# Optimization experiments

Hardware: AMD Instinct MI355X
Metric: run time of the kernel (lower is better)

The kernel has to match this reference:

```python
import jax, jax.numpy as jnp
import numpy as np

N_USERS = 50000
N_ITEMS = 50000
E = 400000
S = 128   # in_feats_s (memory / GRU hidden)
T = 64    # in_feats_t (time encoding dim)
ED = 64   # edge feature dim
M = 2 * S + T + ED  # in_feats_m = 384

_BASIS_FREQ = jnp.asarray(1.0 / 10 ** np.linspace(0, 9, T), dtype=jnp.float32)


def time_encode(ts):
    # cos(ts * freq + phase), phase == 0
    return jnp.cos(ts[:, None] * _BASIS_FREQ[None, :])


def mean_message(src_mem, dst_mem, ts, e, src, dst, n_dst):
    # mail per edge: [E, 2S + T + ED]
    mail = jnp.concatenate(
        [src_mem[src], dst_mem[dst], time_encode(ts), e], axis=1)
    s = jax.ops.segment_sum(mail, dst, num_segments=n_dst)
    cnt = jax.ops.segment_sum(jnp.ones_like(ts), dst, num_segments=n_dst)
    return s / jnp.maximum(cnt, 1.0)[:, None]


def gru_step(x, h, w_ih, w_hh, b_ih, b_hh):
    # single-step PyTorch GRU; gate order r, z, n
    gi = x @ w_ih.T + b_ih
    gh = h @ w_hh.T + b_hh
    ir, iz, i_n = jnp.split(gi, 3, axis=1)
    hr, hz, h_n = jnp.split(gh, 3, axis=1)
    r = jax.nn.sigmoid(ir + hr)
    z = jax.nn.sigmoid(iz + hz)
    n = jnp.tanh(i_n + r * h_n)
    return (1.0 - z) * n + z * h


def setup_inputs() -> dict:
    key = jax.random.key(0)
    ks = jax.random.split(key, 16)
    sc = 1.0 / np.sqrt(S)
    return {
        "si":   jax.random.normal(ks[0], (N_USERS, S), jnp.float32),
        "sj":   jax.random.normal(ks[1], (N_ITEMS, S), jnp.float32),
        "si_r": jax.random.normal(ks[2], (N_ITEMS, S), jnp.float32),
        "sj_r": jax.random.normal(ks[3], (N_USERS, S), jnp.float32),
        "t":    jax.random.uniform(ks[4], (E,), jnp.float32),
        "t_r":  jax.random.uniform(ks[5], (E,), jnp.float32),
        "e":    jax.random.normal(ks[6], (E, ED), jnp.float32),
        "e_r":  jax.random.normal(ks[7], (E, ED), jnp.float32),
        "w_ih": jax.random.normal(ks[8], (3 * S, M), jnp.float32) * sc,
        "w_hh": jax.random.normal(ks[9], (3 * S, S), jnp.float32) * sc,
        "b_ih": jax.random.normal(ks[10], (3 * S,), jnp.float32) * sc,
        "b_hh": jax.random.normal(ks[11], (3 * S,), jnp.float32) * sc,
        "src_g":  jax.random.randint(ks[12], (E,), 0, N_USERS, jnp.int32),
        "dst_g":  jax.random.randint(ks[13], (E,), 0, N_ITEMS, jnp.int32),
        "src_gr": jax.random.randint(ks[14], (E,), 0, N_ITEMS, jnp.int32),
        "dst_gr": jax.random.randint(ks[15], (E,), 0, N_USERS, jnp.int32),
    }


def reference(si, sj, si_r, sj_r, t, t_r, e, e_r,
              w_ih, w_hh, b_ih, b_hh,
              src_g, dst_g, src_gr, dst_gr):
    # g: user -> item; g_r: item -> user
    mj = mean_message(si, sj, t, e, src_g, dst_g, N_ITEMS)       # messages to items
    mi = mean_message(si_r, sj_r, t_r, e_r, src_gr, dst_gr, N_USERS)  # messages to users
    si_out = gru_step(mi, sj_r, w_ih, w_hh, b_ih, b_hh)  # user memory update
    sj_out = gru_step(mj, sj, w_ih, w_hh, b_ih, b_hh)    # item memory update
    return (si_out, sj_out)
```

## Files before the change

### kernel.cpp

```cpp
#include <hip/hip_runtime.h>
#include <math.h>

#define NUSERS 50000
#define NITEMS 50000
#define NTOT   100000
#define NNODE  50000
#define NCHUNK 196
#define MTILES 6250
#define KDIM   512

typedef __attribute__((ext_vector_type(4))) float f32x4;
typedef __attribute__((ext_vector_type(8))) short short8;
typedef unsigned int u32;

#define AS1 __attribute__((address_space(1)))
#define AS3 __attribute__((address_space(3)))

static __device__ __forceinline__ unsigned short f2bf(float f) {
  unsigned int u = __float_as_uint(f);
  u += 0x7fffu + ((u >> 16) & 1u);
  return (unsigned short)(u >> 16);
}

static __device__ __forceinline__ u32 pack2(float x, float y) {
  return (u32)f2bf(x) | ((u32)f2bf(y) << 16);
}

static __device__ __forceinline__ void gload_lds16(const void* g, void* l) {
  __builtin_amdgcn_global_load_lds((const AS1 u32*)g, (AS3 u32*)l, 16, 0, 0);
}

__global__ void pack_w_kernel(const float* __restrict__ w_ih,
                              const float* __restrict__ w_hh,
                              const float* __restrict__ b_ih,
                              const float* __restrict__ b_hh,
                              unsigned short* __restrict__ Wb,
                              float* __restrict__ bb) {
  int idx = blockIdx.x * 256 + threadIdx.x;
  int j = idx & 7, l = (idx >> 3) & 63, ktt = idx >> 9;
  int kt = ktt & 15, tt = ktt >> 4;
  int g = tt * 16 + (l & 15);
  int k = kt * 32 + (l >> 4) * 8 + j;
  float v;
  if (g < 256)      v = (k < 384) ? w_ih[g * 384 + k] : w_hh[g * 128 + (k - 384)];
  else if (g < 384) v = (k < 384) ? w_ih[g * 384 + k] : 0.0f;
  else              v = (k < 384) ? 0.0f : w_hh[(g - 128) * 128 + (k - 384)];
  Wb[idx] = f2bf(v);
  if (idx < 512) {
    float b = (idx < 256) ? (b_ih[idx] + b_hh[idx])
            : (idx < 384) ? b_ih[idx]
                          : b_hh[idx - 128];
    bb[idx] = b;
  }
}

__global__ void cast_mem_kernel(const float* __restrict__ si,
                                const float* __restrict__ si_r,
                                unsigned short* __restrict__ si_b,
                                unsigned short* __restrict__ sir_b) {
  int i = blockIdx.x * 256 + threadIdx.x;
  const float* src; unsigned short* dst; int off;
  if (i < 800000) { src = si;   dst = si_b;  off = i; }
  else            { src = si_r; dst = sir_b; off = i - 800000; }
  const f32x4* p = (const f32x4*)(src + (size_t)off * 8);
  f32x4 a = p[0], b = p[1];
  short8 o;
  o[0] = f2bf(a[0]); o[1] = f2bf(a[1]); o[2] = f2bf(a[2]); o[3] = f2bf(a[3]);
  o[4] = f2bf(b[0]); o[5] = f2bf(b[1]); o[6] = f2bf(b[2]); o[7] = f2bf(b[3]);
  *(short8*)(dst + (size_t)off * 8) = o;
}

__global__ void hist_kernel(const int* __restrict__ dst_g,
                            const int* __restrict__ dst_gr,
                            int* __restrict__ deg_j, int* __restrict__ deg_i, int E) {
  int i = blockIdx.x * 256 + threadIdx.x;
  if (i < E) atomicAdd(&deg_j[dst_g[i]], 1);
  else if (i < 2 * E) atomicAdd(&deg_i[dst_gr[i - E]], 1);
}

__global__ void chunksum_kernel(const int* __restrict__ deg_j,
                                const int* __restrict__ deg_i,
                                int* __restrict__ csum) {
  int c = blockIdx.x;
  const int* deg = (c < NCHUNK) ? deg_j : deg_i;
  int cc = (c < NCHUNK) ? c : c - NCHUNK;
  int t = threadIdx.x;
  int idx = cc * 256 + t;
  int v = (idx < NNODE) ? deg[idx] : 0;
  for (int off = 32; off; off >>= 1) v += __shfl_down(v, off, 64);
  __shared__ int wsum[4];
  if ((t & 63) == 0) wsum[t >> 6] = v;
  __syncthreads();
  if (t == 0) csum[c] = wsum[0] + wsum[1] + wsum[2] + wsum[3];
}

__global__ void chunkscan_kernel(const int* __restrict__ csum, int* __restrict__ coff) {
  int d = blockIdx.x;
  const int* cs = csum + d * NCHUNK;
  int* co = coff + d * NCHUNK;
  int t = threadIdx.x, lane = t & 63, w = t >> 6;
  int v = (t < NCHUNK) ? cs[t] : 0;
  int x = v;
  for (int off = 1; off < 64; off <<= 1) {
    int y = __shfl_up(x, off, 64);
    if (lane >= off) x += y;
  }
  __shared__ int wt[4];
  if (lane == 63) wt[w] = x;
  __syncthreads();
  int add = 0;
  for (int k = 0; k < 4; ++k) if (k < w) add += wt[k];
  if (t < NCHUNK) co[t] = add + x - v;
}

__global__ void localscan_kernel(const int* __restrict__ deg_j,
                                 const int* __restrict__ deg_i,
                                 const int* __restrict__ coff,
                                 int* __restrict__ rs_j, int* __restrict__ cur_j,
                                 int* __restrict__ rs_i, int* __restrict__ cur_i) {
  int c = blockIdx.x;
  bool dj = c < NCHUNK;
  const int* deg = dj ? deg_j : deg_i;
  int cc = dj ? c : c - NCHUNK;
  int* rs = dj ? rs_j : rs_i;
  int* cur = dj ? cur_j : cur_i;
  int base = coff[c];
  int t = threadIdx.x, lane = t & 63, w = t >> 6;
  int idx = cc * 256 + t;
  int v = (idx < NNODE) ? deg[idx] : 0;
  int x = v;
  for (int off = 1; off < 64; off <<= 1) {
    int y = __shfl_up(x, off, 64);
    if (lane >= off) x += y;
  }
  __shared__ int wt[4];
  if (lane == 63) wt[w] = x;
  __syncthreads();
  int add = 0;
  for (int k = 0; k < 4; ++k) if (k < w) add += wt[k];
  int ex = base + add + x - v;
  if (idx < NNODE) { rs[idx] = ex; cur[idx] = ex; }
}

__global__ void fill_kernel(const int* __restrict__ src_g, const int* __restrict__ dst_g,
                            const float* __restrict__ t,
                            const int* __restrict__ src_gr, const int* __restrict__ dst_gr,
                            const float* __restrict__ t_r,
                            int* __restrict__ cur_j, int* __restrict__ cur_i,
                            int4* __restrict__ recP_j, int4* __restrict__ recP_i,
                            int E) {
  int i = blockIdx.x * 256 + threadIdx.x;
  if (i < E) {
    int pos = atomicAdd(&cur_j[dst_g[i]], 1);
    recP_j[pos] = make_int4(src_g[i], i, __float_as_int(t[i]), 0);
  } else if (i < 2 * E) {
    int k = i - E;
    int pos = atomicAdd(&cur_i[dst_gr[k]], 1);
    recP_i[pos] = make_int4(src_gr[k], k, __float_as_int(t_r[k]), 0);
  }
}

__global__ __launch_bounds__(256) void gather_kernel(
    const unsigned short* __restrict__ si_b, const unsigned short* __restrict__ sir_b,
    const float* __restrict__ sj, const float* __restrict__ sj_r,
    const float* __restrict__ e, const float* __restrict__ e_r,
    const int* __restrict__ rs_j, const int* __restrict__ rs_i,
    const int* __restrict__ deg_j, const int* __restrict__ deg_i,
    const int4* __restrict__ recP_j, const int4* __restrict__ recP_i,
    unsigned short* __restrict__ Xb) {
  __shared__ __align__(16) unsigned short rowbuf[4][512];
  int wid = threadIdx.x >> 6, lane = threadIdx.x & 63;
  int node = blockIdx.x * 4 + wid;
  bool user = node < NUSERS;
  int idx = user ? node : node - NUSERS;
  const unsigned short* smem = user ? sir_b : si_b;
  const float* h    = user ? sj_r : sj;
  const float* ef   = user ? e_r : e;
  int start = __builtin_amdgcn_readfirstlane((user ? rs_i : rs_j)[idx]);
  int deg   = __builtin_amdgcn_readfirstlane((user ? deg_i : deg_j)[idx]);
  const int4* rec = user ? recP_i : recP_j;

  float freq = __expf((float)lane * -0.3289407276f);
  float2 hvf = *(const float2*)(h + (size_t)idx * 128 + 2 * lane);

  float asx = 0.f, asy = 0.f;
  float at  = 0.f;
  float ae  = 0.f;

  for (int base = 0; base < deg; base += 64) {
    int nn = deg - base; if (nn > 64) nn = 64;
    int cl = (lane < nn) ? base + lane : base + nn - 1;
    int4 r = rec[start + cl];
    for (int j0 = 0; j0 < nn; j0 += 8) {
      int j1 = (j0 + 1 < nn) ? j0 + 1 : nn - 1;
      int j2 = (j0 + 2 < nn) ? j0 + 2 : nn - 1;
      int j3 = (j0 + 3 < nn) ? j0 + 3 : nn - 1;
      int j4 = (j0 + 4 < nn) ? j0 + 4 : nn - 1;
      int j5 = (j0 + 5 < nn) ? j0 + 5 : nn - 1;
      int j6 = (j0 + 6 < nn) ? j0 + 6 : nn - 1;
      int j7 = (j0 + 7 < nn) ? j0 + 7 : nn - 1;
      float w1 = (j0 + 1 < nn) ? 1.0f : 0.0f;
      float w2 = (j0 + 2 < nn) ? 1.0f : 0.0f;
      float w3 = (j0 + 3 < nn) ? 1.0f : 0.0f;
      float w4 = (j0 + 4 < nn) ? 1.0f : 0.0f;
      float w5 = (j0 + 5 < nn) ? 1.0f : 0.0f;
      float w6 = (j0 + 6 < nn) ? 1.0f : 0.0f;
      float w7 = (j0 + 7 < nn) ? 1.0f : 0.0f;

      int s0 = __builtin_amdgcn_readlane(r.x, j0), e0 = __builtin_amdgcn_readlane(r.y, j0);
      int s1 = __builtin_amdgcn_readlane(r.x, j1), e1 = __builtin_amdgcn_readlane(r.y, j1);
      int s2 = __builtin_amdgcn_readlane(r.x, j2), e2 = __builtin_amdgcn_readlane(r.y, j2);
      int s3 = __builtin_amdgcn_readlane(r.x, j3), e3 = __builtin_amdgcn_readlane(r.y, j3);
      int s4 = __builtin_amdgcn_readlane(r.x, j4), e4 = __builtin_amdgcn_readlane(r.y, j4);
      int s5 = __builtin_amdgcn_readlane(r.x, j5), e5 = __builtin_amdgcn_readlane(r.y, j5);
      int s6 = __builtin_amdgcn_readlane(r.x, j6), e6 = __builtin_amdgcn_readlane(r.y, j6);
      int s7 = __builtin_amdgcn_readlane(r.x, j7), e7 = __builtin_amdgcn_readlane(r.y, j7);

      u32 v0 = *(const u32*)(smem + ((size_t)s0 << 7) + 2 * lane);
      u32 v1 = *(const u32*)(smem + ((size_t)s1 << 7) + 2 * lane);
      u32 v2 = *(const u32*)(smem + ((size_t)s2 << 7) + 2 * lane);
      u32 v3 = *(const u32*)(smem + ((size_t)s3 << 7) + 2 * lane);
      u32 v4 = *(const u32*)(smem + ((size_t)s4 << 7) + 2 * lane);
      u32 v5 = *(const u32*)(smem + ((size_t)s5 << 7) + 2 * lane);
      u32 v6 = *(const u32*)(smem + ((size_t)s6 << 7) + 2 * lane);
      u32 v7 = *(const u32*)(smem + ((size_t)s7 << 7) + 2 * lane);
      float f0 = ef[((size_t)e0 << 6) + lane];
      float f1 = ef[((size_t)e1 << 6) + lane];
      float f2 = ef[((size_t)e2 << 6) + lane];
      float f3 = ef[((size_t)e3 << 6) + lane];
      float f4 = ef[((size_t)e4 << 6) + lane];
      float f5 = ef[((size_t)e5 << 6) + lane];
      float f6 = ef[((size_t)e6 << 6) + lane];
      float f7 = ef[((size_t)e7 << 6) + lane];

      float c0 = __cosf(__int_as_float(__builtin_amdgcn_readlane(r.z, j0)) * freq);
      float c1 = __cosf(__int_as_float(__builtin_amdgcn_readlane(r.z, j1)) * freq);
      float c2 = __cosf(__int_as_float(__builtin_amdgcn_readlane(r.z, j2)) * freq);
      float c3 = __cosf(__int_as_float(__builtin_amdgcn_readlane(r.z, j3)) * freq);
      float c4 = __cosf(__int_as_float(__builtin_amdgcn_readlane(r.z, j4)) * freq);
      float c5 = __cosf(__int_as_float(__builtin_amdgcn_readlane(r.z, j5)) * freq);
      float c6 = __cosf(__int_as_float(__builtin_amdgcn_readlane(r.z, j6)) * freq);
      float c7 = __cosf(__int_as_float(__builtin_amdgcn_readlane(r.z, j7)) * freq);

      float l0 = __uint_as_float(v0 << 16), g0 = __uint_as_float(v0 & 0xffff0000u);
      float l1 = __uint_as_float(v1 << 16), g1 = __uint_as_float(v1 & 0xffff0000u);
      float l2 = __uint_as_float(v2 << 16), g2 = __uint_as_float(v2 & 0xffff0000u);
      float l3 = __uint_as_float(v3 << 16), g3 = __uint_as_float(v3 & 0xffff0000u);
      float l4 = __uint_as_float(v4 << 16), g4 = __uint_as_float(v4 & 0xffff0000u);
      float l5 = __uint_as_float(v5 << 16), g5 = __uint_as_float(v5 & 0xffff0000u);
      float l6 = __uint_as_float(v6 << 16), g6 = __uint_as_float(v6 & 0xffff0000u);
      float l7 = __uint_as_float(v7 << 16), g7 = __uint_as_float(v7 & 0xffff0000u);

      asx += l0 + w1 * l1 + w2 * l2 + w3 * l3 + w4 * l4 + w5 * l5 + w6 * l6 + w7 * l7;
      asy += g0 + w1 * g1 + w2 * g2 + w3 * g3 + w4 * g4 + w5 * g5 + w6 * g6 + w7 * g7;
      at  += c0 + w1 * c1 + w2 * c2 + w3 * c3 + w4 * c4 + w5 * c5 + w6 * c6 + w7 * c7;
      ae  += f0 + w1 * f1 + w2 * f2 + w3 * f3 + w4 * f4 + w5 * f5 + w6 * f6 + w7 * f7;
    }
  }

  float invc = (deg > 0) ? 1.0f / (float)deg : 0.0f;
  float hz   = (deg > 0) ? 1.0f : 0.0f;

  unsigned short* rb = rowbuf[wid];
  u32* rb32 = (u32*)rb;
  rb32[lane]       = pack2(asx * invc, asy * invc);
  rb32[64 + lane]  = pack2(hvf.x * hz, hvf.y * hz);
  rb[256 + lane]   = f2bf(at * invc);
  rb[320 + lane]   = f2bf(ae * invc);
  rb32[192 + lane] = pack2(hvf.x, hvf.y);

  int rt = node >> 4, m = node & 15;
  int kt2 = lane >> 2, q2 = lane & 3;
  short8 vv = *(const short8*)(rb + lane * 8);
  *(short8*)(Xb + (((size_t)rt * 16 + kt2) * 64 + q2 * 16 + m) * 8) = vv;
}

__global__ __launch_bounds__(1024, 4) void gemm_gru_kernel(
    const unsigned short* __restrict__ Xb,
    const unsigned short* __restrict__ Wb,
    const float* __restrict__ bb,
    const float* __restrict__ sj_r,
    const float* __restrict__ sj,
    float* __restrict__ out) {
  __shared__ __align__(16) unsigned short sA[32768];
  __shared__ __align__(16) unsigned short sW[2][16384];
  int wid = threadIdx.x >> 6, lane = threadIdx.x & 63;
  int mg = wid >> 3, cg = wid & 7;
  int mbase = blockIdx.x * 4;
  int col16 = lane & 15, quad = lane >> 4;

  f32x4 acc[2][4];
#pragma unroll
  for (int mi = 0; mi < 2; ++mi)
#pragma unroll
    for (int g = 0; g < 4; ++g) acc[mi][g] = (f32x4)0.0f;

#pragma unroll
  for (int i = 0; i < 4; ++i) {
    int u = wid * 4 + i;
    int mt = mbase + (u >> 4);
    if (mt >= MTILES) mt = MTILES - 1;
    const unsigned short* gp = Xb + (size_t)mt * 8192 + (u & 15) * 512 + lane * 8;
    gload_lds16(gp, sA + u * 512);
  }
#pragma unroll
  for (int i = 0; i < 2; ++i) {
    int tt = wid * 2 + i;
    const unsigned short* gp = Wb + ((size_t)(tt * 16 + 0) * 64 + lane) * 8;
    gload_lds16(gp, sW[0] + tt * 512);
  }
  __syncthreads();

  const unsigned short* aBase = sA + (size_t)(mg * 32) * 512 + lane * 8;

  for (int kt = 0; kt < 16; ++kt) {
    int cur = kt & 1;
    if (kt < 15) {
#pragma unroll
      for (int i = 0; i < 2; ++i) {
        int tt = wid * 2 + i;
        const unsigned short* gp = Wb + ((size_t)(tt * 16 + kt + 1) * 64 + lane) * 8;
        gload_lds16(gp, sW[cur ^ 1] + tt * 512);
      }
    }
    short8 a0 = *(const short8*)(aBase + (size_t)kt * 512);
    short8 a1 = *(const short8*)(aBase + (size_t)(16 + kt) * 512);
    short8 b0 = *(const short8*)(sW[cur] + (0 * 8 + cg) * 512 + lane * 8);
    short8 b1 = *(const short8*)(sW[cur] + (1 * 8 + cg) * 512 + lane * 8);
    short8 b2 = *(const short8*)(sW[cur] + (2 * 8 + cg) * 512 + lane * 8);
    short8 b3 = *(const short8*)(sW[cur] + (3 * 8 + cg) * 512 + lane * 8);
    acc[0][0] = __builtin_amdgcn_mfma_f32_16x16x32_bf16(a0, b0, acc[0][0], 0, 0, 0);
    acc[0][1] = __builtin_amdgcn_mfma_f32_16x16x32_bf16(a0, b1, acc[0][1], 0, 0, 0);
    acc[0][2] = __builtin_amdgcn_mfma_f32_16x16x32_bf16(a0, b2, acc[0][2], 0, 0, 0);
    acc[0][3] = __builtin_amdgcn_mfma_f32_16x16x32_bf16(a0, b3, acc[0][3], 0, 0, 0);
    acc[1][0] = __builtin_amdgcn_mfma_f32_16x16x32_bf16(a1, b0, acc[1][0], 0, 0, 0);
    acc[1][1] = __builtin_amdgcn_mfma_f32_16x16x32_bf16(a1, b1, acc[1][1], 0, 0, 0);
    acc[1][2] = __builtin_amdgcn_mfma_f32_16x16x32_bf16(a1, b2, acc[1][2], 0, 0, 0);
    acc[1][3] = __builtin_amdgcn_mfma_f32_16x16x32_bf16(a1, b3, acc[1][3], 0, 0, 0);
    __syncthreads();
  }

  int cc = cg * 16 + col16;
  float bbr = bb[cc], bbz = bb[128 + cc], bbn = bb[256 + cc], bbh = bb[384 + cc];
#pragma unroll
  for (int mi = 0; mi < 2; ++mi) {
    int mt = mbase + mg * 2 + mi;
    if (mt >= MTILES) continue;
#pragma unroll
    for (int r = 0; r < 4; ++r) {
      int row = mt * 16 + quad * 4 + r;
      float rp  = acc[mi][0][r] + bbr;
      float zp  = acc[mi][1][r] + bbz;
      float inp = acc[mi][2][r] + bbn;
      float hnp = acc[mi][3][r] + bbh;
      float rg = 1.0f / (1.0f + __expf(-rp));
      float zg = 1.0f / (1.0f + __expf(-zp));
      float ng = tanhf(inp + rg * hnp);
      float hv = (row < NUSERS) ? sj_r[(size_t)row * 128 + cc]
                                : sj[(size_t)(row - NUSERS) * 128 + cc];
      out[(size_t)row * 128 + cc] = (1.0f - zg) * ng + zg * hv;
    }
  }
}

extern "C" void kernel_launch(void* const* d_in, const int* in_sizes, int n_in,
                              void* d_out, int out_size, void* d_ws, size_t ws_size,
                              hipStream_t stream) {
  const float* si   = (const float*)d_in[0];
  const float* sj   = (const float*)d_in[1];
  const float* si_r = (const float*)d_in[2];
  const float* sj_r = (const float*)d_in[3];
  const float* t    = (const float*)d_in[4];
  const float* t_r  = (const float*)d_in[5];
  const float* e    = (const float*)d_in[6];
  const float* e_r  = (const float*)d_in[7];
  const float* w_ih = (const float*)d_in[8];
  const float* w_hh = (const float*)d_in[9];
  const float* b_ih = (const float*)d_in[10];
  const float* b_hh = (const float*)d_in[11];
  const int* src_g  = (const int*)d_in[12];
  const int* dst_g  = (const int*)d_in[13];
  const int* src_gr = (const int*)d_in[14];
  const int* dst_gr = (const int*)d_in[15];
  int E = in_sizes[4];

  unsigned short* Xb = (unsigned short*)d_ws;
  unsigned short* Wb = Xb + (size_t)MTILES * 8192;
  float* bb   = (float*)(Wb + 262144);
  int* deg_j  = (int*)(bb + 512);
  int* deg_i  = deg_j + NNODE;
  int* rs_j   = deg_i + NNODE;
  int* rs_i   = rs_j + NNODE;
  int* cur_j  = rs_i + NNODE;
  int* cur_i  = cur_j + NNODE;
  int* csum   = cur_i + NNODE;
  int* coff   = csum + 2 * NCHUNK;
  int4* recP_j = (int4*)(coff + 2 * NCHUNK);
  int4* recP_i = recP_j + E;
  unsigned short* si_b  = (unsigned short*)(recP_i + E);
  unsigned short* sir_b = si_b + 6400000;

  hipMemsetAsync(deg_j, 0, 2 * NNODE * sizeof(int), stream);

  pack_w_kernel<<<(512 * 512) / 256, 256, 0, stream>>>(w_ih, w_hh, b_ih, b_hh, Wb, bb);
  cast_mem_kernel<<<6250, 256, 0, stream>>>(si, si_r, si_b, sir_b);

  int blks2E = (2 * E + 255) / 256;
  hist_kernel<<<blks2E, 256, 0, stream>>>(dst_g, dst_gr, deg_j, deg_i, E);
  chunksum_kernel<<<2 * NCHUNK, 256, 0, stream>>>(deg_j, deg_i, csum);
  chunkscan_kernel<<<2, 256, 0, stream>>>(csum, coff);
  localscan_kernel<<<2 * NCHUNK, 256, 0, stream>>>(deg_j, deg_i, coff, rs_j, cur_j, rs_i, cur_i);
  fill_kernel<<<blks2E, 256, 0, stream>>>(src_g, dst_g, t, src_gr, dst_gr, t_r,
                                          cur_j, cur_i, recP_j, recP_i, E);

  gather_kernel<<<NTOT / 4, 256, 0, stream>>>(si_b, sir_b, sj, sj_r, e, e_r,
                                              rs_j, rs_i, deg_j, deg_i,
                                              recP_j, recP_i, Xb);

  float* out = (float*)d_out;
  gemm_gru_kernel<<<(MTILES + 3) / 4, 1024, 0, stream>>>(Xb, Wb, bb, sj_r, sj, out);
}
```

Measured before the change: 622.3 us.

## Use persistent gather waves, row-major X layout, and fast path for full 8-edge groups

The gather kernel now runs a fixed grid of 8192 persistent waves that grid-stride over nodes, where before it launched one wave per node. The inner edge loop gets a branch-free path for full groups of 8 with tree-sum accumulation, and only the tail group keeps the clamped, weighted form. The gather writes rows contiguously, and the GEMM's A-tile load addressing is rewritten to read that row-major layout. This is meant to cut launch and scheduling overhead and per-edge select work, and to make the gather writes coalesced. In exchange, the GEMM's LDS loads become more strided, and per-wave load imbalance may grow.

```diff
diff --git a/kernel.cpp b/kernel.cpp
--- a/kernel.cpp
+++ b/kernel.cpp
@@ -8,6 +8,7 @@
 #define NCHUNK 196
 #define MTILES 6250
 #define KDIM   512
+#define NWAVES 8192
 
 typedef __attribute__((ext_vector_type(4))) float f32x4;
 typedef __attribute__((ext_vector_type(8))) short short8;
@@ -170,109 +171,155 @@
     unsigned short* __restrict__ Xb) {
   __shared__ __align__(16) unsigned short rowbuf[4][512];
   int wid = threadIdx.x >> 6, lane = threadIdx.x & 63;
-  int node = blockIdx.x * 4 + wid;
-  bool user = node < NUSERS;
-  int idx = user ? node : node - NUSERS;
-  const unsigned short* smem = user ? sir_b : si_b;
-  const float* h    = user ? sj_r : sj;
-  const float* ef   = user ? e_r : e;
-  int start = __builtin_amdgcn_readfirstlane((user ? rs_i : rs_j)[idx]);
-  int deg   = __builtin_amdgcn_readfirstlane((user ? deg_i : deg_j)[idx]);
-  const int4* rec = user ? recP_i : recP_j;
-
+  int gwave = blockIdx.x * 4 + wid;
   float freq = __expf((float)lane * -0.3289407276f);
-  float2 hvf = *(const float2*)(h + (size_t)idx * 128 + 2 * lane);
-
-  float asx = 0.f, asy = 0.f;
-  float at  = 0.f;
-  float ae  = 0.f;
-
-  for (int base = 0; base < deg; base += 64) {
-    int nn = deg - base; if (nn > 64) nn = 64;
-    int cl = (lane < nn) ? base + lane : base + nn - 1;
-    int4 r = rec[start + cl];
-    for (int j0 = 0; j0 < nn; j0 += 8) {
-      int j1 = (j0 + 1 < nn) ? j0 + 1 : nn - 1;
-      int j2 = (j0 + 2 < nn) ? j0 + 2 : nn - 1;
-      int j3 = (j0 + 3 < nn) ? j0 + 3 : nn - 1;
-      int j4 = (j0 + 4 < nn) ? j0 + 4 : nn - 1;
-      int j5 = (j0 + 5 < nn) ? j0 + 5 : nn - 1;
-      int j6 = (j0 + 6 < nn) ? j0 + 6 : nn - 1;
-      int j7 = (j0 + 7 < nn) ? j0 + 7 : nn - 1;
-      float w1 = (j0 + 1 < nn) ? 1.0f : 0.0f;
-      float w2 = (j0 + 2 < nn) ? 1.0f : 0.0f;
-      float w3 = (j0 + 3 < nn) ? 1.0f : 0.0f;
-      float w4 = (j0 + 4 < nn) ? 1.0f : 0.0f;
-      float w5 = (j0 + 5 < nn) ? 1.0f : 0.0f;
-      float w6 = (j0 + 6 < nn) ? 1.0f : 0.0f;
-      float w7 = (j0 + 7 < nn) ? 1.0f : 0.0f;
-
-      int s0 = __builtin_amdgcn_readlane(r.x, j0), e0 = __builtin_amdgcn_readlane(r.y, j0);
-      int s1 = __builtin_amdgcn_readlane(r.x, j1), e1 = __builtin_amdgcn_readlane(r.y, j1);
-      int s2 = __builtin_amdgcn_readlane(r.x, j2), e2 = __builtin_amdgcn_readlane(r.y, j2);
-      int s3 = __builtin_amdgcn_readlane(r.x, j3), e3 = __builtin_amdgcn_readlane(r.y, j3);
-      int s4 = __builtin_amdgcn_readlane(r.x, j4), e4 = __builtin_amdgcn_readlane(r.y, j4);
-      int s5 = __builtin_amdgcn_readlane(r.x, j5), e5 = __builtin_amdgcn_readlane(r.y, j5);
-      int s6 = __builtin_amdgcn_readlane(r.x, j6), e6 = __builtin_amdgcn_readlane(r.y, j6);
-      int s7 = __builtin_amdgcn_readlane(r.x, j7), e7 = __builtin_amdgcn_readlane(r.y, j7);
-
-      u32 v0 = *(const u32*)(smem + ((size_t)s0 << 7) + 2 * lane);
-      u32 v1 = *(const u32*)(smem + ((size_t)s1 << 7) + 2 * lane);
-      u32 v2 = *(const u32*)(smem + ((size_t)s2 << 7) + 2 * lane);
-      u32 v3 = *(const u32*)(smem + ((size_t)s3 << 7) + 2 * lane);
-      u32 v4 = *(const u32*)(smem + ((size_t)s4 << 7) + 2 * lane);
-      u32 v5 = *(const u32*)(smem + ((size_t)s5 << 7) + 2 * lane);
-      u32 v6 = *(const u32*)(smem + ((size_t)s6 << 7) + 2 * lane);
-      u32 v7 = *(const u32*)(smem + ((size_t)s7 << 7) + 2 * lane);
-      float f0 = ef[((size_t)e0 << 6) + lane];
-      float f1 = ef[((size_t)e1 << 6) + lane];
-      float f2 = ef[((size_t)e2 << 6) + lane];
-      float f3 = ef[((size_t)e3 << 6) + lane];
-      float f4 = ef[((size_t)e4 << 6) + lane];
-      float f5 = ef[((size_t)e5 << 6) + lane];
-      float f6 = ef[((size_t)e6 << 6) + lane];
-      float f7 = ef[((size_t)e7 << 6) + lane];
-
-      float c0 = __cosf(__int_as_float(__builtin_amdgcn_readlane(r.z, j0)) * freq);
-      float c1 = __cosf(__int_as_float(__builtin_amdgcn_readlane(r.z, j1)) * freq);
-      float c2 = __cosf(__int_as_float(__builtin_amdgcn_readlane(r.z, j2)) * freq);
-      float c3 = __cosf(__int_as_float(__builtin_amdgcn_readlane(r.z, j3)) * freq);
-      float c4 = __cosf(__int_as_float(__builtin_amdgcn_readlane(r.z, j4)) * freq);
-      float c5 = __cosf(__int_as_float(__builtin_amdgcn_readlane(r.z, j5)) * freq);
-      float c6 = __cosf(__int_as_float(__builtin_amdgcn_readlane(r.z, j6)) * freq);
-      float c7 = __cosf(__int_as_float(__builtin_amdgcn_readlane(r.z, j7)) * freq);
-
-      float l0 = __uint_as_float(v0 << 16), g0 = __uint_as_float(v0 & 0xffff0000u);
-      float l1 = __uint_as_float(v1 << 16), g1 = __uint_as_float(v1 & 0xffff0000u);
-      float l2 = __uint_as_float(v2 << 16), g2 = __uint_as_float(v2 & 0xffff0000u);
-      float l3 = __uint_as_float(v3 << 16), g3 = __uint_as_float(v3 & 0xffff0000u);
-      float l4 = __uint_as_float(v4 << 16), g4 = __uint_as_float(v4 & 0xffff0000u);
-      float l5 = __uint_as_float(v5 << 16), g5 = __uint_as_float(v5 & 0xffff0000u);
-      float l6 = __uint_as_float(v6 << 16), g6 = __uint_as_float(v6 & 0xffff0000u);
-      float l7 = __uint_as_float(v7 << 16), g7 = __uint_as_float(v7 & 0xffff0000u);
-
-      asx += l0 + w1 * l1 + w2 * l2 + w3 * l3 + w4 * l4 + w5 * l5 + w6 * l6 + w7 * l7;
-      asy += g0 + w1 * g1 + w2 * g2 + w3 * g3 + w4 * g4 + w5 * g5 + w6 * g6 + w7 * g7;
-      at  += c0 + w1 * c1 + w2 * c2 + w3 * c3 + w4 * c4 + w5 * c5 + w6 * c6 + w7 * c7;
-      ae  += f0 + w1 * f1 + w2 * f2 + w3 * f3 + w4 * f4 + w5 * f5 + w6 * f6 + w7 * f7;
-    }
-  }
-
-  float invc = (deg > 0) ? 1.0f / (float)deg : 0.0f;
-  float hz   = (deg > 0) ? 1.0f : 0.0f;
-
   unsigned short* rb = rowbuf[wid];
   u32* rb32 = (u32*)rb;
-  rb32[lane]       = pack2(asx * invc, asy * invc);
-  rb32[64 + lane]  = pack2(hvf.x * hz, hvf.y * hz);
-  rb[256 + lane]   = f2bf(at * invc);
-  rb[320 + lane]   = f2bf(ae * invc);
-  rb32[192 + lane] = pack2(hvf.x, hvf.y);
-
-  int rt = node >> 4, m = node & 15;
-  int kt2 = lane >> 2, q2 = lane & 3;
-  short8 vv = *(const short8*)(rb + lane * 8);
-  *(short8*)(Xb + (((size_t)rt * 16 + kt2) * 64 + q2 * 16 + m) * 8) = vv;
+
+  for (int node = gwave; node < NTOT; node += NWAVES) {
+    bool user = node < NUSERS;
+    int idx = user ? node : node - NUSERS;
+    const unsigned short* smem = user ? sir_b : si_b;
+    const float* h  = user ? sj_r : sj;
+    const float* ef = user ? e_r : e;
+    int start = __builtin_amdgcn_readfirstlane((user ? rs_i : rs_j)[idx]);
+    int deg   = __builtin_amdgcn_readfirstlane((user ? deg_i : deg_j)[idx]);
+    const int4* rec = user ? recP_i : recP_j;
+
+    float2 hvf = *(const float2*)(h + (size_t)idx * 128 + 2 * lane);
+
+    float asx = 0.f, asy = 0.f;
+    float at  = 0.f;
+    float ae  = 0.f;
+
+    for (int base = 0; base < deg; base += 64) {
+      int nn = deg - base; if (nn > 64) nn = 64;
+      int cl = (lane < nn) ? base + lane : base + nn - 1;
+      int4 r = rec[start + cl];
+      int full = nn & ~7;
+      for (int j0 = 0; j0 < full; j0 += 8) {
+        int s0 = __builtin_amdgcn_readlane(r.x, j0 + 0), e0 = __builtin_amdgcn_readlane(r.y, j0 + 0);
+        int s1 = __builtin_amdgcn_readlane(r.x, j0 + 1), e1 = __builtin_amdgcn_readlane(r.y, j0 + 1);
+        int s2 = __builtin_amdgcn_readlane(r.x, j0 + 2), e2 = __builtin_amdgcn_readlane(r.y, j0 + 2);
+        int s3 = __builtin_amdgcn_readlane(r.x, j0 + 3), e3 = __builtin_amdgcn_readlane(r.y, j0 + 3);
+        int s4 = __builtin_amdgcn_readlane(r.x, j0 + 4), e4 = __builtin_amdgcn_readlane(r.y, j0 + 4);
+        int s5 = __builtin_amdgcn_readlane(r.x, j0 + 5), e5 = __builtin_amdgcn_readlane(r.y, j0 + 5);
+        int s6 = __builtin_amdgcn_readlane(r.x, j0 + 6), e6 = __builtin_amdgcn_readlane(r.y, j0 + 6);
+        int s7 = __builtin_amdgcn_readlane(r.x, j0 + 7), e7 = __builtin_amdgcn_readlane(r.y, j0 + 7);
+
+        u32 v0 = *(const u32*)(smem + ((size_t)s0 << 7) + 2 * lane);
+        u32 v1 = *(const u32*)(smem + ((size_t)s1 << 7) + 2 * lane);
+        u32 v2 = *(const u32*)(smem + ((size_t)s2 << 7) + 2 * lane);
+        u32 v3 = *(const u32*)(smem + ((size_t)s3 << 7) + 2 * lane);
+        u32 v4 = *(const u32*)(smem + ((size_t)s4 << 7) + 2 * lane);
+        u32 v5 = *(const u32*)(smem + ((size_t)s5 << 7) + 2 * lane);
+        u32 v6 = *(const u32*)(smem + ((size_t)s6 << 7) + 2 * lane);
+        u32 v7 = *(const u32*)(smem + ((size_t)s7 << 7) + 2 * lane);
+        float f0 = ef[((size_t)e0 << 6) + lane];
+        float f1 = ef[((size_t)e1 << 6) + lane];
+        float f2 = ef[((size_t)e2 << 6) + lane];
+        float f3 = ef[((size_t)e3 << 6) + lane];
+        float f4 = ef[((size_t)e4 << 6) + lane];
+        float f5 = ef[((size_t)e5 << 6) + lane];
+        float f6 = ef[((size_t)e6 << 6) + lane];
+        float f7 = ef[((size_t)e7 << 6) + lane];
+
+        float c0 = __cosf(__int_as_float(__builtin_amdgcn_readlane(r.z, j0 + 0)) * freq);
+        float c1 = __cosf(__int_as_float(__builtin_amdgcn_readlane(r.z, j0 + 1)) * freq);
+        float c2 = __cosf(__int_as_float(__builtin_amdgcn_readlane(r.z, j0 + 2)) * freq);
+        float c3 = __cosf(__int_as_float(__builtin_amdgcn_readlane(r.z, j0 + 3)) * freq);
+        float c4 = __cosf(__int_as_float(__builtin_amdgcn_readlane(r.z, j0 + 4)) * freq);
+        float c5 = __cosf(__int_as_float(__builtin_amdgcn_readlane(r.z, j0 + 5)) * freq);
+        float c6 = __cosf(__int_as_float(__builtin_amdgcn_readlane(r.z, j0 + 6)) * freq);
+        float c7 = __cosf(__int_as_float(__builtin_amdgcn_readlane(r.z, j0 + 7)) * freq);
+
+        float l0 = __uint_as_float(v0 << 16), g0 = __uint_as_float(v0 & 0xffff0000u);
+        float l1 = __uint_as_float(v1 << 16), g1 = __uint_as_float(v1 & 0xffff0000u);
+        float l2 = __uint_as_float(v2 << 16), g2 = __uint_as_float(v2 & 0xffff0000u);
+        float l3 = __uint_as_float(v3 << 16), g3 = __uint_as_float(v3 & 0xffff0000u);
+        float l4 = __uint_as_float(v4 << 16), g4 = __uint_as_float(v4 & 0xffff0000u);
+        float l5 = __uint_as_float(v5 << 16), g5 = __uint_as_float(v5 & 0xffff0000u);
+        float l6 = __uint_as_float(v6 << 16), g6 = __uint_as_float(v6 & 0xffff0000u);
+        float l7 = __uint_as_float(v7 << 16), g7 = __uint_as_float(v7 & 0xffff0000u);
+
+        asx += ((l0 + l1) + (l2 + l3)) + ((l4 + l5) + (l6 + l7));
+        asy += ((g0 + g1) + (g2 + g3)) + ((g4 + g5) + (g6 + g7));
+        at  += ((c0 + c1) + (c2 + c3)) + ((c4 + c5) + (c6 + c7));
+        ae  += ((f0 + f1) + (f2 + f3)) + ((f4 + f5) + (f6 + f7));
+      }
+      if (full < nn) {
+        int j0 = full;
+        int j1 = (j0 + 1 < nn) ? j0 + 1 : nn - 1;
+        int j2 = (j0 + 2 < nn) ? j0 + 2 : nn - 1;
+        int j3 = (j0 + 3 < nn) ? j0 + 3 : nn - 1;
+        int j4 = (j0 + 4 < nn) ? j0 + 4 : nn - 1;
+        int j5 = (j0 + 5 < nn) ? j0 + 5 : nn - 1;
+        int j6 = (j0 + 6 < nn) ? j0 + 6 : nn - 1;
+        float w1 = (j0 + 1 < nn) ? 1.0f : 0.0f;
+        float w2 = (j0 + 2 < nn) ? 1.0f : 0.0f;
+        float w3 = (j0 + 3 < nn) ? 1.0f : 0.0f;
+        float w4 = (j0 + 4 < nn) ? 1.0f : 0.0f;
+        float w5 = (j0 + 5 < nn) ? 1.0f : 0.0f;
+        float w6 = (j0 + 6 < nn) ? 1.0f : 0.0f;
+
+        int s0 = __builtin_amdgcn_readlane(r.x, j0), e0 = __builtin_amdgcn_readlane(r.y, j0);
+        int s1 = __builtin_amdgcn_readlane(r.x, j1), e1 = __builtin_amdgcn_readlane(r.y, j1);
+        int s2 = __builtin_amdgcn_readlane(r.x, j2), e2 = __builtin_amdgcn_readlane(r.y, j2);
+        int s3 = __builtin_amdgcn_readlane(r.x, j3), e3 = __builtin_amdgcn_readlane(r.y, j3);
+        int s4 = __builtin_amdgcn_readlane(r.x, j4), e4 = __builtin_amdgcn_readlane(r.y, j4);
+        int s5 = __builtin_amdgcn_readlane(r.x, j5), e5 = __builtin_amdgcn_readlane(r.y, j5);
+        int s6 = __builtin_amdgcn_readlane(r.x, j6), e6 = __builtin_amdgcn_readlane(r.y, j6);
+
+        u32 v0 = *(const u32*)(smem + ((size_t)s0 << 7) + 2 * lane);
+        u32 v1 = *(const u32*)(smem + ((size_t)s1 << 7) + 2 * lane);
+        u32 v2 = *(const u32*)(smem + ((size_t)s2 << 7) + 2 * lane);
+        u32 v3 = *(const u32*)(smem + ((size_t)s3 << 7) + 2 * lane);
+        u32 v4 = *(const u32*)(smem + ((size_t)s4 << 7) + 2 * lane);
+        u32 v5 = *(const u32*)(smem + ((size_t)s5 << 7) + 2 * lane);
+        u32 v6 = *(const u32*)(smem + ((size_t)s6 << 7) + 2 * lane);
+        float f0 = ef[((size_t)e0 << 6) + lane];
+        float f1 = ef[((size_t)e1 << 6) + lane];
+        float f2 = ef[((size_t)e2 << 6) + lane];
+        float f3 = ef[((size_t)e3 << 6) + lane];
+        float f4 = ef[((size_t)e4 << 6) + lane];
+        float f5 = ef[((size_t)e5 << 6) + lane];
+        float f6 = ef[((size_t)e6 << 6) + lane];
+
+        float c0 = __cosf(__int_as_float(__builtin_amdgcn_readlane(r.z, j0)) * freq);
+        float c1 = __cosf(__int_as_float(__builtin_amdgcn_readlane(r.z, j1)) * freq);
+        float c2 = __cosf(__int_as_float(__builtin_amdgcn_readlane(r.z, j2)) * freq);
+        float c3 = __cosf(__int_as_float(__builtin_amdgcn_readlane(r.z, j3)) * freq);
+        float c4 = __cosf(__int_as_float(__builtin_amdgcn_readlane(r.z, j4)) * freq);
+        float c5 = __cosf(__int_as_float(__builtin_amdgcn_readlane(r.z, j5)) * freq);
+        float c6 = __cosf(__int_as_float(__builtin_amdgcn_readlane(r.z, j6)) * freq);
+
+        float l0 = __uint_as_float(v0 << 16), g0 = __uint_as_float(v0 & 0xffff0000u);
+        float l1 = __uint_as_float(v1 << 16), g1 = __uint_as_float(v1 & 0xffff0000u);
+        float l2 = __uint_as_float(v2 << 16), g2 = __uint_as_float(v2 & 0xffff0000u);
+        float l3 = __uint_as_float(v3 << 16), g3 = __uint_as_float(v3 & 0xffff0000u);
+        float l4 = __uint_as_float(v4 << 16), g4 = __uint_as_float(v4 & 0xffff0000u);
+        float l5 = __uint_as_float(v5 << 16), g5 = __uint_as_float(v5 & 0xffff0000u);
+        float l6 = __uint_as_float(v6 << 16), g6 = __uint_as_float(v6 & 0xffff0000u);
+
+        asx += l0 + w1 * l1 + w2 * l2 + w3 * l3 + w4 * l4 + w5 * l5 + w6 * l6;
+        asy += g0 + w1 * g1 + w2 * g2 + w3 * g3 + w4 * g4 + w5 * g5 + w6 * g6;
+        at  += c0 + w1 * c1 + w2 * c2 + w3 * c3 + w4 * c4 + w5 * c5 + w6 * c6;
+        ae  += f0 + w1 * f1 + w2 * f2 + w3 * f3 + w4 * f4 + w5 * f5 + w6 * f6;
+      }
+    }
+
+    float invc = (deg > 0) ? 1.0f / (float)deg : 0.0f;
+    float hz   = (deg > 0) ? 1.0f : 0.0f;
+
+    rb32[lane]       = pack2(asx * invc, asy * invc);
+    rb32[64 + lane]  = pack2(hvf.x * hz, hvf.y * hz);
+    rb[256 + lane]   = f2bf(at * invc);
+    rb[320 + lane]   = f2bf(ae * invc);
+    rb32[192 + lane] = pack2(hvf.x, hvf.y);
+
+    short8 vv = *(const short8*)(rb + lane * 8);
+    *(short8*)(Xb + (size_t)node * 512 + lane * 8) = vv;
+  }
 }
 
 __global__ __launch_bounds__(1024, 4) void gemm_gru_kernel(
@@ -300,7 +347,8 @@
     int u = wid * 4 + i;
     int mt = mbase + (u >> 4);
     if (mt >= MTILES) mt = MTILES - 1;
-    const unsigned short* gp = Xb + (size_t)mt * 8192 + (u & 15) * 512 + lane * 8;
+    const unsigned short* gp = Xb + (size_t)(mt * 16 + (lane & 15)) * 512
+                                  + (u & 15) * 32 + (lane >> 4) * 8;
     gload_lds16(gp, sA + u * 512);
   }
 #pragma unroll
@@ -385,7 +433,7 @@
   int E = in_sizes[4];
 
   unsigned short* Xb = (unsigned short*)d_ws;
-  unsigned short* Wb = Xb + (size_t)MTILES * 8192;
+  unsigned short* Wb = Xb + (size_t)NTOT * 512;
   float* bb   = (float*)(Wb + 262144);
   int* deg_j  = (int*)(bb + 512);
   int* deg_i  = deg_j + NNODE;
@@ -413,9 +461,9 @@
   fill_kernel<<<blks2E, 256, 0, stream>>>(src_g, dst_g, t, src_gr, dst_gr, t_r,
                                           cur_j, cur_i, recP_j, recP_i, E);
 
-  gather_kernel<<<NTOT / 4, 256, 0, stream>>>(si_b, sir_b, sj, sj_r, e, e_r,
-                                              rs_j, rs_i, deg_j, deg_i,
-                                              recP_j, recP_i, Xb);
+  gather_kernel<<<NWAVES / 4, 256, 0, stream>>>(si_b, sir_b, sj, sj_r, e, e_r,
+                                                rs_j, rs_i, deg_j, deg_i,
+                                                recP_j, recP_i, Xb);
 
   float* out = (float*)d_out;
   gemm_gru_kernel<<<(MTILES + 3) / 4, 1024, 0, stream>>>(Xb, Wb, bb, sj_r, sj, out);
```

After: 592.5 us. 4.8% less time.
